# Performance work log

Measured on AMD Instinct MI355X. Metric: run time of the kernel, lower is better.

## Reference

```python
import jax, jax.numpy as jnp
import numpy as np

S_LEN = 1024; HIDDEN = 2048; VOCAB = 32000; DFF = 6144
NK = 8; NV = 16; DK = 128; DV = 128; CONV_K = 4
CONV_DIM = 2 * NK * DK + NV * DV  # 4096
NQ = 16; NKV = 2; HD = 128; MAX_KV = 4096; SP = 512; CHUNK = 64


def silu(x):
    return x * jax.nn.sigmoid(x)


def rmsnorm(x, w, eps=1e-6):
    xf = x.astype(jnp.float32)
    return (xf * jax.lax.rsqrt(jnp.mean(xf * xf, -1, keepdims=True) + eps)) * w


def gated_rmsnorm(x, z, w, eps=1e-6):
    xf = x.astype(jnp.float32) * silu(z.astype(jnp.float32))
    return (xf * jax.lax.rsqrt(jnp.mean(xf * xf, -1, keepdims=True) + eps)) * w


def rotate_half(x):
    a, b = jnp.split(x, 2, -1)
    return jnp.concatenate([-b, a], -1)


def chunk_gated_delta_rule(q, k, v, g, beta, init_state, chunk=CHUNK):
    # q,k: [B,S,H,Dk]; v: [B,S,H,Dv]; g,beta: [B,S,H]; init_state: [B,H,Dk,Dv]
    q = q / jnp.sqrt(jnp.sum(q * q, -1, keepdims=True) + 1e-6)  # qk l2norm
    k = k / jnp.sqrt(jnp.sum(k * k, -1, keepdims=True) + 1e-6)
    tr = lambda x: x.transpose(0, 2, 1, 3).astype(jnp.float32)
    q, k, v = tr(q), tr(k), tr(v)
    g = g.transpose(0, 2, 1).astype(jnp.float32)
    beta = beta.transpose(0, 2, 1).astype(jnp.float32)
    B, H, S, Dk = q.shape
    Dv = v.shape[-1]
    N = S // chunk  # S is a multiple of chunk here (no padding needed)
    q = q * Dk ** -0.5
    rc = lambda x: x.reshape(B, H, N, chunk, x.shape[-1])
    q, k, v = rc(q), rc(k), rc(v)
    g = jnp.cumsum(g.reshape(B, H, N, chunk), -1)  # cumulative log-decay within chunk
    beta = beta.reshape(B, H, N, chunk)
    kb = k * beta[..., None]
    vb = v * beta[..., None]
    ii = jnp.arange(chunk)
    lower = ii[:, None] >= ii[None, :]
    strict = ii[:, None] > ii[None, :]
    decay = jnp.where(lower, jnp.exp(g[..., :, None] - g[..., None, :]), 0.0)
    # strictly-lower A; T = (I - A)^{-1} (exact triangular solve == converged Neumann series)
    A = -jnp.where(strict, jnp.einsum('bhnik,bhnjk->bhnij', kb, k) * decay, 0.0)
    eye = jnp.eye(chunk, dtype=jnp.float32)
    T = jax.scipy.linalg.solve_triangular(eye - A, jnp.broadcast_to(eye, A.shape), lower=True)
    w = jnp.einsum('bhnij,bhnjd->bhnid', T, vb)
    kc = jnp.einsum('bhnij,bhnjd->bhnid', T, kb * jnp.exp(g)[..., None])
    mv = lambda x: jnp.moveaxis(x, 2, 0)

    def step(state, xs):
        qi, ki, wi, kci, gi, di = xs
        attn = jnp.where(lower, jnp.einsum('bhik,bhjk->bhij', qi, ki) * di, 0.0)
        v_new = wi - jnp.einsum('bhik,bhkd->bhid', kci, state)
        out = jnp.einsum('bhik,bhkd->bhid', qi * jnp.exp(gi)[..., None], state) \
            + jnp.einsum('bhij,bhjd->bhid', attn, v_new)
        gl = gi[..., -1]
        kd = ki * jnp.exp(gl[..., None] - gi)[..., None]
        state = state * jnp.exp(gl)[..., None, None] + jnp.einsum('bhik,bhid->bhkd', kd, v_new)
        return state, out

    final, outs = jax.lax.scan(step, init_state.astype(jnp.float32),
                               (mv(q), mv(k), mv(w), mv(kc), mv(g), mv(decay)))
    out = jnp.moveaxis(outs, 0, 2).reshape(B, H, S, Dv).transpose(0, 2, 1, 3)  # [B,S,H,Dv]
    return out, final


def mlp(x, gw, uw, dw):
    return (silu(x @ gw) * (x @ uw)) @ dw


def model_forward(input_ids, start_pos, rope_cos, rope_sin, attn_mask, conv_state, rec_state,
                  key_cache, value_cache, embed_w, dl_ln_w, dl_qkv_w, conv_w, conv_b, dl_z_w,
                  dl_b_w, dl_a_w, A_log, dt_bias, dn_norm_w, dl_out_w, dl_post_ln_w, dl_gate_w,
                  dl_up_w, dl_down_w, al_ln_w, q_w, q_norm_w, k_w, k_norm_w, v_w, o_w,
                  al_post_ln_w, al_gate_w, al_up_w, al_down_w, final_norm_w, lm_head_w):
    B, S = input_ids.shape
    hidden = embed_w[input_ids]
    # ---------------- DeltaNet (linear attention) layer ----------------
    res = hidden
    x = rmsnorm(hidden, dl_ln_w)
    mixed = (x @ dl_qkv_w).transpose(0, 2, 1)             # [B, CONV_DIM, S]
    padded = jnp.concatenate([conv_state, mixed], -1)      # [B, CONV_DIM, K+S]
    L = padded.shape[-1] - (CONV_K - 1)
    conv = conv_b[:, None] + sum(conv_w[:, kk][:, None] * padded[:, :, kk:kk + L]
                                 for kk in range(CONV_K))  # depthwise conv1d
    mixed = silu(conv[:, :, -S:]).transpose(0, 2, 1)
    new_conv = padded[:, :, -CONV_K:]
    kd = NK * DK
    qq = mixed[..., :kd].reshape(B, S, NK, DK)
    kk_ = mixed[..., kd:2 * kd].reshape(B, S, NK, DK)
    vv = mixed[..., 2 * kd:].reshape(B, S, NV, DV)
    z = (x @ dl_z_w).reshape(B, S, NV, DV)
    beta = jax.nn.sigmoid(x @ dl_b_w)
    a = (x @ dl_a_w).astype(jnp.float32)
    g = -jnp.exp(A_log.astype(jnp.float32)) * jax.nn.softplus(a + dt_bias)
    rep = NV // NK
    qq = jnp.repeat(qq, rep, axis=2)
    kk_ = jnp.repeat(kk_, rep, axis=2)
    core, new_rec = chunk_gated_delta_rule(qq, kk_, vv, g, beta, rec_state)
    core = gated_rmsnorm(core.reshape(-1, DV), z.reshape(-1, DV), dn_norm_w).reshape(B, S, NV * DV)
    hidden = res + core @ dl_out_w
    hidden = hidden + mlp(rmsnorm(hidden, dl_post_ln_w), dl_gate_w, dl_up_w, dl_down_w)
    # ---------------- Full attention layer (gated GQA, KV-cache scatter) ----------------
    res = hidden
    x = rmsnorm(hidden, al_ln_w)
    qg = (x @ q_w).reshape(B, S, NQ, 2 * HD)
    query, gate = jnp.split(qg, 2, -1)
    gate = gate.reshape(B, S, NQ * HD)
    query = rmsnorm(query, q_norm_w).transpose(0, 2, 1, 3)               # [B,NQ,S,HD]
    key_new = rmsnorm((x @ k_w).reshape(B, S, NKV, HD), k_norm_w).transpose(0, 2, 1, 3)
    value_new = (x @ v_w).reshape(B, S, NKV, HD).transpose(0, 2, 1, 3)
    c = rope_cos[:, None]
    sn = rope_sin[:, None]
    query = query * c + rotate_half(query) * sn
    key_new = key_new * c + rotate_half(key_new) * sn
    new_kc = jax.lax.dynamic_update_slice(key_cache, key_new, (0, 0, start_pos, 0))
    new_vc = jax.lax.dynamic_update_slice(value_cache, value_new, (0, 0, start_pos, 0))
    ng = NQ // NKV
    k_rep = jnp.repeat(new_kc, ng, axis=1)
    v_rep = jnp.repeat(new_vc, ng, axis=1)
    scores = jnp.einsum('bhsd,bhtd->bhst', query, k_rep) * HD ** -0.5 + attn_mask
    probs = jax.nn.softmax(scores.astype(jnp.float32), -1).astype(query.dtype)
    ao = jnp.einsum('bhst,bhtd->bhsd', probs, v_rep).transpose(0, 2, 1, 3).reshape(B, S, NQ * HD)
    ao = ao * jax.nn.sigmoid(gate)
    hidden = res + ao @ o_w
    hidden = hidden + mlp(rmsnorm(hidden, al_post_ln_w), al_gate_w, al_up_w, al_down_w)
    logits = rmsnorm(hidden, final_norm_w) @ lm_head_w
    return logits, new_conv, new_rec, new_kc, new_vc


def setup_inputs():
    key = jax.random.key(0)
    ks = iter(jax.random.split(key, 64))
    def rn(shape, s=0.02):
        return jax.random.normal(next(ks), shape, jnp.float32) * s
    input_ids = jax.random.randint(next(ks), (1, S_LEN), 0, VOCAB)
    inv = 1.0 / (10000.0 ** (jnp.arange(0, HD, 2, dtype=jnp.float32) / HD))
    pos = jnp.arange(SP, SP + S_LEN, dtype=jnp.float32)
    fr = pos[:, None] * inv[None, :]
    emb = jnp.concatenate([fr, fr], -1)
    rope_cos = jnp.cos(emb)[None]
    rope_sin = jnp.sin(emb)[None]
    qpos = SP + jnp.arange(S_LEN)
    kpos = jnp.arange(MAX_KV)
    attn_mask = jnp.where(kpos[None, :] <= qpos[:, None], 0.0, -1e9).astype(jnp.float32)[None, None]
    return dict(
        input_ids=input_ids, seq_len=S_LEN, start_pos=SP,
        rope_cos=rope_cos, rope_sin=rope_sin, attn_mask=attn_mask,
        conv_state=rn((1, CONV_DIM, CONV_K), 1.0), rec_state=rn((1, NV, DK, DV), 1.0),
        key_cache=rn((1, NKV, MAX_KV, HD), 1.0), value_cache=rn((1, NKV, MAX_KV, HD), 1.0),
        embed_w=rn((VOCAB, HIDDEN)), dl_ln_w=jnp.ones(HIDDEN),
        dl_qkv_w=rn((HIDDEN, CONV_DIM)), conv_w=rn((CONV_DIM, CONV_K), 0.3),
        conv_b=rn((CONV_DIM,)), dl_z_w=rn((HIDDEN, NV * DV)),
        dl_b_w=rn((HIDDEN, NV)), dl_a_w=rn((HIDDEN, NV)),
        A_log=jnp.log(jnp.linspace(1.0, 8.0, NV)), dt_bias=rn((NV,), 0.1),
        dn_norm_w=jnp.ones(DV), dl_out_w=rn((NV * DV, HIDDEN)),
        dl_post_ln_w=jnp.ones(HIDDEN), dl_gate_w=rn((HIDDEN, DFF)),
        dl_up_w=rn((HIDDEN, DFF)), dl_down_w=rn((DFF, HIDDEN)),
        al_ln_w=jnp.ones(HIDDEN), q_w=rn((HIDDEN, NQ * HD * 2)), q_norm_w=jnp.ones(HD),
        k_w=rn((HIDDEN, NKV * HD)), k_norm_w=jnp.ones(HD), v_w=rn((HIDDEN, NKV * HD)),
        o_w=rn((NQ * HD, HIDDEN)), al_post_ln_w=jnp.ones(HIDDEN),
        al_gate_w=rn((HIDDEN, DFF)), al_up_w=rn((HIDDEN, DFF)), al_down_w=rn((DFF, HIDDEN)),
        final_norm_w=jnp.ones(HIDDEN), lm_head_w=rn((HIDDEN, VOCAB)))


def reference(input_ids, seq_len, start_pos, rope_cos, rope_sin, attn_mask, conv_state,
              rec_state, key_cache, value_cache, embed_w, dl_ln_w, dl_qkv_w, conv_w, conv_b,
              dl_z_w, dl_b_w, dl_a_w, A_log, dt_bias, dn_norm_w, dl_out_w, dl_post_ln_w,
              dl_gate_w, dl_up_w, dl_down_w, al_ln_w, q_w, q_norm_w, k_w, k_norm_w, v_w, o_w,
              al_post_ln_w, al_gate_w, al_up_w, al_down_w, final_norm_w, lm_head_w):
    del seq_len  # unused in original forward body (padding bookkeeping only)
    return model_forward(input_ids, start_pos, rope_cos, rope_sin, attn_mask, conv_state,
                         rec_state, key_cache, value_cache, embed_w, dl_ln_w, dl_qkv_w, conv_w,
                         conv_b, dl_z_w, dl_b_w, dl_a_w, A_log, dt_bias, dn_norm_w, dl_out_w,
                         dl_post_ln_w, dl_gate_w, dl_up_w, dl_down_w, al_ln_w, q_w, q_norm_w,
                         k_w, k_norm_w, v_w, o_w, al_post_ln_w, al_gate_w, al_up_w, al_down_w,
                         final_norm_w, lm_head_w)
```

## Files before the change

### kernel.cpp

```cpp
#include <hip/hip_runtime.h>
#include <math.h>

#define S_LEN 1024
#define HIDN  2048
#define NVH   16
#define CDIM  4096
#define MAXKV 4096
#define SP    512

typedef __attribute__((ext_vector_type(4))) float f32x4v;
typedef _Float16 f16x8 __attribute__((ext_vector_type(8)));
typedef unsigned short ushort_t;

__device__ __forceinline__ unsigned int pack2h(float a, float b) {
  auto h = __builtin_amdgcn_cvt_pkrtz(a, b);
  return __builtin_bit_cast(unsigned int, h);
}
__device__ __forceinline__ ushort_t h16(float x) {
  auto v = __builtin_amdgcn_cvt_pkrtz(x, x);
  return (ushort_t)__builtin_bit_cast(unsigned int, v);
}

template<int TM, bool ACC, bool FS>
__global__ __launch_bounds__(256) void gemm_f16(const float* __restrict__ A,
    const float* A2, const float* __restrict__ B,
    float* __restrict__ C, int M, int N, int K) {
  constexpr int MI = TM / 32;
  constexpr int AF = TM / 8;
  __shared__ unsigned int Al[4][TM][4];
  __shared__ unsigned int Bl[4][128][4];
  const int tid = threadIdx.x;
  const int gm = M / TM;
  const int nwg = gridDim.x;
  const int q = nwg >> 3, r = nwg & 7;
  const int xcd = blockIdx.x & 7, ii = blockIdx.x >> 3;
  const int lin = (xcd < r) ? (xcd * (q + 1) + ii)
                            : (r * (q + 1) + (xcd - r) * q + ii);
  const int m0 = (lin % gm) * TM;
  const int n0 = (lin / gm) * 128;
  const int wave = tid >> 6, lane = tid & 63;
  const int wm = (wave >> 1) * (TM / 2), wn = (wave & 1) * 64;
  const int lr = lane & 15, lg = lane >> 4;
  const int am  = (TM == 128) ? (tid >> 1) : (tid >> 2);
  const int akb = (TM == 128) ? ((tid & 1) * 2) : (tid & 3);
  const int bn = tid & 127, bkb = (tid >> 7) * 2;
  const float* Ap  = A + (size_t)(m0 + am) * K + akb * 8;
  const float* A2p = A2 + (size_t)(m0 + am) * K + akb * 8;
  const float* Bp = B + (size_t)(bkb * 8) * N + n0 + bn;
  float ar[AF], ar2[FS ? AF : 1], br[16];
  f32x4v acc[MI][4];
  #pragma unroll
  for (int i = 0; i < MI; ++i)
    #pragma unroll
    for (int j = 0; j < 4; ++j)
      #pragma unroll
      for (int r2 = 0; r2 < 4; ++r2) acc[i][j][r2] = 0.f;
  const int NT = K >> 5;
  #pragma unroll
  for (int q2 = 0; q2 < AF / 4; ++q2)
    *(float4*)&ar[q2 * 4] = *(const float4*)(Ap + q2 * 4);
  if (FS) {
    #pragma unroll
    for (int q2 = 0; q2 < AF / 4; ++q2)
      *(float4*)&ar2[q2 * 4] = *(const float4*)(A2p + q2 * 4);
  }
  #pragma unroll
  for (int j = 0; j < 16; ++j) br[j] = Bp[(size_t)j * N];
  for (int t = 0; t < NT; ++t) {
    __syncthreads();
    float av[AF];
    #pragma unroll
    for (int u = 0; u < AF; ++u) {
      float g = ar[u];
      av[u] = FS ? (g / (1.f + expf(-g))) * ar2[u] : g;
    }
    *(uint4*)&Al[akb][am][0] = make_uint4(
        pack2h(av[0], av[1]), pack2h(av[2], av[3]),
        pack2h(av[4], av[5]), pack2h(av[6], av[7]));
    if (TM == 128) {
      *(uint4*)&Al[akb + 1][am][0] = make_uint4(
          pack2h(av[8], av[9]), pack2h(av[10], av[11]),
          pack2h(av[12], av[13]), pack2h(av[14], av[15]));
    }
    *(uint4*)&Bl[bkb][bn][0] = make_uint4(
        pack2h(br[0], br[1]), pack2h(br[2], br[3]),
        pack2h(br[4], br[5]), pack2h(br[6], br[7]));
    *(uint4*)&Bl[bkb + 1][bn][0] = make_uint4(
        pack2h(br[8], br[9]), pack2h(br[10], br[11]),
        pack2h(br[12], br[13]), pack2h(br[14], br[15]));
    if (t + 1 < NT) {
      Ap += 32; A2p += 32; Bp += (size_t)32 * N;
      #pragma unroll
      for (int q2 = 0; q2 < AF / 4; ++q2)
        *(float4*)&ar[q2 * 4] = *(const float4*)(Ap + q2 * 4);
      if (FS) {
        #pragma unroll
        for (int q2 = 0; q2 < AF / 4; ++q2)
          *(float4*)&ar2[q2 * 4] = *(const float4*)(A2p + q2 * 4);
      }
      #pragma unroll
      for (int j = 0; j < 16; ++j) br[j] = Bp[(size_t)j * N];
    }
    __syncthreads();
    f16x8 af[MI], bfr[4];
    #pragma unroll
    for (int mi = 0; mi < MI; ++mi)
      af[mi] = *(const f16x8*)&Al[lg][wm + mi * 16 + lr][0];
    #pragma unroll
    for (int ni = 0; ni < 4; ++ni)
      bfr[ni] = *(const f16x8*)&Bl[lg][wn + ni * 16 + lr][0];
    #pragma unroll
    for (int mi = 0; mi < MI; ++mi)
      #pragma unroll
      for (int ni = 0; ni < 4; ++ni)
        acc[mi][ni] = __builtin_amdgcn_mfma_f32_16x16x32_f16(
            af[mi], bfr[ni], acc[mi][ni], 0, 0, 0);
  }
  #pragma unroll
  for (int mi = 0; mi < MI; ++mi) {
    #pragma unroll
    for (int ni = 0; ni < 4; ++ni) {
      const int rr = m0 + wm + mi * 16 + lg * 4;
      const int cc = n0 + wn + ni * 16 + lr;
      #pragma unroll
      for (int r2 = 0; r2 < 4; ++r2) {
        float* cp = C + (size_t)(rr + r2) * N + cc;
        if (ACC) *cp += acc[mi][ni][r2];
        else     *cp = acc[mi][ni][r2];
      }
    }
  }
}

__global__ __launch_bounds__(256) void embed_k(const int* __restrict__ ids,
    const float* __restrict__ emb, float* __restrict__ hid) {
  int t = blockIdx.x * 256 + threadIdx.x;
  int s = t >> 9;
  int c4 = (t & 511) * 4;
  *(float4*)(hid + (size_t)s * HIDN + c4) =
      *(const float4*)(emb + (size_t)ids[s] * HIDN + c4);
}

__global__ __launch_bounds__(256) void rmsnorm_k(const float* __restrict__ in,
    const float* __restrict__ w, float* __restrict__ out) {
  const int row = blockIdx.x;
  const float* ip = in + (size_t)row * HIDN;
  float ss = 0.f;
  for (int c = threadIdx.x * 4; c < HIDN; c += 1024) {
    float4 v = *(const float4*)(ip + c);
    ss += v.x * v.x + v.y * v.y + v.z * v.z + v.w * v.w;
  }
  #pragma unroll
  for (int o = 32; o > 0; o >>= 1) ss += __shfl_down(ss, o, 64);
  __shared__ float sred[4];
  if ((threadIdx.x & 63) == 0) sred[threadIdx.x >> 6] = ss;
  __syncthreads();
  float tot = sred[0] + sred[1] + sred[2] + sred[3];
  float sc = 1.f / sqrtf(tot * (1.f / HIDN) + 1e-6f);
  for (int c = threadIdx.x * 4; c < HIDN; c += 1024) {
    float4 v = *(const float4*)(ip + c);
    float4 o = make_float4(v.x * sc * w[c], v.y * sc * w[c + 1],
                           v.z * sc * w[c + 2], v.w * sc * w[c + 3]);
    *(float4*)(out + (size_t)row * HIDN + c) = o;
  }
}

__global__ __launch_bounds__(256) void newconv_k(const float* __restrict__ mixed,
                                                 float* __restrict__ nc) {
  int t = blockIdx.x * 256 + threadIdx.x;
  int c = t >> 2, kk = t & 3;
  nc[t] = mixed[(size_t)(1020 + kk) * CDIM + c];
}

__global__ __launch_bounds__(256) void conv_k(const float* __restrict__ mixed,
    const float* __restrict__ cstate, const float* __restrict__ cw,
    const float* __restrict__ cb, float* __restrict__ convo) {
  int idx = blockIdx.x * 256 + threadIdx.x;
  int c = idx & (CDIM - 1);
  int s = idx >> 12;
  float acc = cb[c];
  #pragma unroll
  for (int kk = 0; kk < 4; ++kk) {
    int j = s + 1 + kk;
    float pv = (j < 4) ? cstate[c * 4 + j] : mixed[(size_t)(j - 4) * CDIM + c];
    acc = fmaf(cw[c * 4 + kk], pv, acc);
  }
  convo[(size_t)s * CDIM + c] = acc / (1.f + expf(-acc));
}

__global__ __launch_bounds__(128) void qknorm_k(const float* __restrict__ convo,
    float* __restrict__ qn, float* __restrict__ kn) {
  const int b = blockIdx.x;
  const int h8 = b & 7, s = b >> 3;
  const int d = threadIdx.x;
  float qv = convo[(size_t)s * CDIM + h8 * 128 + d];
  float kv = convo[(size_t)s * CDIM + 1024 + h8 * 128 + d];
  __shared__ float sred[4];
  float pq = qv * qv, pk = kv * kv;
  #pragma unroll
  for (int o = 32; o > 0; o >>= 1) { pq += __shfl_down(pq, o, 64); pk += __shfl_down(pk, o, 64); }
  if ((d & 63) == 0) { sred[d >> 6] = pq; sred[2 + (d >> 6)] = pk; }
  __syncthreads();
  float sq = sred[0] + sred[1], sk = sred[2] + sred[3];
  qn[((size_t)h8 * S_LEN + s) * 128 + d] = qv * (1.f / sqrtf(sq + 1e-6f)) * 0.08838834764831845f;
  kn[((size_t)h8 * S_LEN + s) * 128 + d] = kv * (1.f / sqrtf(sk + 1e-6f));
}

__global__ __launch_bounds__(256) void betag_k(const float* __restrict__ x,
    const float* __restrict__ bw, const float* __restrict__ aw,
    const float* __restrict__ A_log, const float* __restrict__ dt_bias,
    float* __restrict__ beta, float* __restrict__ g) {
  __shared__ float sx[2048];
  __shared__ float rb[16][17], ra[16][17];
  const int s = blockIdx.x;
  for (int c = threadIdx.x; c < HIDN; c += 256) sx[c] = x[(size_t)s * HIDN + c];
  __syncthreads();
  const int h = threadIdx.x & 15, part = threadIdx.x >> 4;
  float accb = 0.f, acca = 0.f;
  for (int j = 0; j < 128; ++j) {
    int k = part * 128 + j;
    float xv = sx[k];
    accb = fmaf(xv, bw[(size_t)k * 16 + h], accb);
    acca = fmaf(xv, aw[(size_t)k * 16 + h], acca);
  }
  rb[part][h] = accb; ra[part][h] = acca;
  __syncthreads();
  if (threadIdx.x < 16) {
    const int hh = threadIdx.x;
    float sb = 0.f, sa = 0.f;
    for (int p = 0; p < 16; ++p) { sb += rb[p][hh]; sa += ra[p][hh]; }
    beta[(size_t)s * 16 + hh] = 1.f / (1.f + expf(-sb));
    float aa = sa + dt_bias[hh];
    float sp = (aa > 20.f) ? aa : log1pf(expf(aa));
    g[(size_t)s * 16 + hh] = -expf(A_log[hh]) * sp;
  }
}

__global__ __launch_bounds__(256) void delta_phase1(
    const float* __restrict__ qn, const float* __restrict__ kn,
    const float* __restrict__ convo, const float* __restrict__ beta,
    const float* __restrict__ g,
    float* __restrict__ Wb, ushort_t* __restrict__ KC16,
    ushort_t* __restrict__ Q16, ushort_t* __restrict__ K16,
    ushort_t* __restrict__ ATT16, float* __restrict__ GCb) {
  __shared__ float sK[64][129];
  __shared__ float sV[64][129];
  __shared__ float sQ[64][129];
  __shared__ float sT[64][64];
  __shared__ float sgc[64], sbeta[64], seg[64], sEgl[64];
  const int blk = blockIdx.x;
  const int n = blk & 15, h = blk >> 4;
  const int hq = h >> 1;
  const int r0 = n * 64;
  const int tid = threadIdx.x;
  const size_t hn = (size_t)h * 16 + n;
  for (int t = tid; t < 2048; t += 256) {
    int i = t >> 5, c4 = (t & 31) * 4;
    float4 kv = *(const float4*)(kn + ((size_t)hq * S_LEN + r0 + i) * 128 + c4);
    float4 qv = *(const float4*)(qn + ((size_t)hq * S_LEN + r0 + i) * 128 + c4);
    float4 vv = *(const float4*)(convo + (size_t)(r0 + i) * CDIM + 2048 + h * 128 + c4);
    sK[i][c4+0]=kv.x; sK[i][c4+1]=kv.y; sK[i][c4+2]=kv.z; sK[i][c4+3]=kv.w;
    sQ[i][c4+0]=qv.x; sQ[i][c4+1]=qv.y; sQ[i][c4+2]=qv.z; sQ[i][c4+3]=qv.w;
    sV[i][c4+0]=vv.x; sV[i][c4+1]=vv.y; sV[i][c4+2]=vv.z; sV[i][c4+3]=vv.w;
  }
  if (tid < 64) sbeta[tid] = beta[(size_t)(r0 + tid) * NVH + h];
  __syncthreads();
  if (tid == 0) {
    float acc = 0.f;
    for (int i = 0; i < 64; ++i) { acc += g[(size_t)(r0 + i) * NVH + h]; sgc[i] = acc; }
  }
  __syncthreads();
  if (tid < 64) {
    seg[tid] = expf(sgc[tid]);
    sEgl[tid] = expf(sgc[63] - sgc[tid]);
  }
  {
    const int ty = tid >> 4, tx = tid & 15;
    float a[4][4] = {};
    #pragma unroll 4
    for (int k = 0; k < 128; ++k) {
      float kr[4], kc_[4];
      #pragma unroll
      for (int di = 0; di < 4; ++di) kr[di] = sK[ty * 4 + di][k];
      #pragma unroll
      for (int dj = 0; dj < 4; ++dj) kc_[dj] = sK[tx * 4 + dj][k];
      #pragma unroll
      for (int di = 0; di < 4; ++di)
        #pragma unroll
        for (int dj = 0; dj < 4; ++dj)
          a[di][dj] = fmaf(kr[di], kc_[dj], a[di][dj]);
    }
    #pragma unroll
    for (int di = 0; di < 4; ++di) {
      int i = ty * 4 + di;
      #pragma unroll
      for (int dj = 0; dj < 4; ++dj) {
        int j = tx * 4 + dj;
        float v;
        if (i > j) v = sbeta[i] * a[di][dj] * expf(sgc[i] - sgc[j]);
        else v = (i == j) ? 1.f : 0.f;
        sT[i][j] = v;
      }
    }
  }
  __syncthreads();
  if (tid < 64) {
    const int c = tid;
    for (int i = 1; i < 64; ++i) {
      if (c <= i) {
        float acc = (c == i) ? 1.f : 0.f;
        for (int j = c; j < i; ++j) acc -= sT[i][j] * sT[j][c];
        sT[i][c] = acc;
      }
    }
  }
  __syncthreads();
  for (int t = tid; t < 1024; t += 256) {
    int i = t >> 4, dg = (t & 15) * 8;
    float aw[8] = {}, ak[8] = {};
    for (int j = 0; j <= i; ++j) {
      float tv = sT[i][j] * sbeta[j];
      float te = tv * seg[j];
      #pragma unroll
      for (int u = 0; u < 8; ++u) {
        aw[u] = fmaf(tv, sV[j][dg + u], aw[u]);
        ak[u] = fmaf(te, sK[j][dg + u], ak[u]);
      }
    }
    float* wp = Wb + (hn * 64 + i) * 128 + dg;
    *(float4*)wp = make_float4(aw[0], aw[1], aw[2], aw[3]);
    *(float4*)(wp + 4) = make_float4(aw[4], aw[5], aw[6], aw[7]);
    uint4 kc = make_uint4(pack2h(-ak[0], -ak[1]), pack2h(-ak[2], -ak[3]),
                          pack2h(-ak[4], -ak[5]), pack2h(-ak[6], -ak[7]));
    *(uint4*)(KC16 + hn * 8192 + (dg >> 3) * 512 + i * 8) = kc;
  }
  for (int t = tid; t < 1024; t += 256) {
    int i = t >> 4, dg = (t & 15) * 8;
    float e = seg[i];
    uint4 qv = make_uint4(
        pack2h(sQ[i][dg] * e, sQ[i][dg + 1] * e),
        pack2h(sQ[i][dg + 2] * e, sQ[i][dg + 3] * e),
        pack2h(sQ[i][dg + 4] * e, sQ[i][dg + 5] * e),
        pack2h(sQ[i][dg + 6] * e, sQ[i][dg + 7] * e));
    *(uint4*)(Q16 + hn * 8192 + (dg >> 3) * 512 + i * 8) = qv;
  }
  for (int t = tid; t < 1024; t += 256) {
    int kv = t & 127, ib = t >> 7;
    int i0 = ib * 8;
    uint4 kk2 = make_uint4(
        pack2h(sK[i0 + 0][kv] * sEgl[i0 + 0], sK[i0 + 1][kv] * sEgl[i0 + 1]),
        pack2h(sK[i0 + 2][kv] * sEgl[i0 + 2], sK[i0 + 3][kv] * sEgl[i0 + 3]),
        pack2h(sK[i0 + 4][kv] * sEgl[i0 + 4], sK[i0 + 5][kv] * sEgl[i0 + 5]),
        pack2h(sK[i0 + 6][kv] * sEgl[i0 + 6], sK[i0 + 7][kv] * sEgl[i0 + 7]));
    *(uint4*)(K16 + hn * 8192 + ib * 1024 + kv * 8) = kk2;
  }
  __syncthreads();
  {
    const int ty = tid >> 4, tx = tid & 15;
    float a[4][4] = {};
    #pragma unroll 4
    for (int k = 0; k < 128; ++k) {
      float qr[4], kc_[4];
      #pragma unroll
      for (int di = 0; di < 4; ++di) qr[di] = sQ[ty * 4 + di][k];
      #pragma unroll
      for (int dj = 0; dj < 4; ++dj) kc_[dj] = sK[tx * 4 + dj][k];
      #pragma unroll
      for (int di = 0; di < 4; ++di)
        #pragma unroll
        for (int dj = 0; dj < 4; ++dj)
          a[di][dj] = fmaf(qr[di], kc_[dj], a[di][dj]);
    }
    #pragma unroll
    for (int di = 0; di < 4; ++di) {
      int i = ty * 4 + di;
      #pragma unroll
      for (int dj = 0; dj < 4; ++dj) {
        int j = tx * 4 + dj;
        float v = 0.f;
        if (i >= j) v = a[di][dj] * expf(sgc[i] - sgc[j]);
        sT[i][j] = v;
      }
    }
  }
  __syncthreads();
  for (int t = tid; t < 512; t += 256) {
    int i = t >> 3, jb = t & 7;
    const float* ap = &sT[i][jb * 8];
    uint4 av = make_uint4(pack2h(ap[0], ap[1]), pack2h(ap[2], ap[3]),
                          pack2h(ap[4], ap[5]), pack2h(ap[6], ap[7]));
    *(uint4*)(ATT16 + hn * 4096 + jb * 512 + i * 8) = av;
  }
  if (tid < 64) GCb[hn * 64 + tid] = sgc[tid];
}

__global__ __launch_bounds__(256) void delta_phase2(
    const ushort_t* __restrict__ KC16, const ushort_t* __restrict__ Q16,
    const ushort_t* __restrict__ K16, const ushort_t* __restrict__ ATT16,
    const float* __restrict__ Wb, const float* __restrict__ GCb,
    const float* __restrict__ rec_state,
    float* __restrict__ core, float* __restrict__ new_rec) {
  __shared__ uint4 bufKC[1024];
  __shared__ uint4 bufQ[1024];
  __shared__ uint4 bufK[1024];
  __shared__ uint4 bufA[512];
  __shared__ uint4 bufS[512];
  __shared__ uint4 bufV[256];
  ushort_t* sKC = (ushort_t*)bufKC;
  ushort_t* sQ6 = (ushort_t*)bufQ;
  ushort_t* sK6 = (ushort_t*)bufK;
  ushort_t* sAT = (ushort_t*)bufA;
  ushort_t* sS  = (ushort_t*)bufS;
  ushort_t* sVn = (ushort_t*)bufV;
  const int h = blockIdx.x >> 2, ds = blockIdx.x & 3;
  const int d0 = ds * 32;
  const int tid = threadIdx.x;
  const int w = tid >> 6;
  const int lane = tid & 63, lr = lane & 15, lg = lane >> 4;
  const int rowS0 = w * 32;
  f32x4v aS[2][2];
  #pragma unroll
  for (int tm = 0; tm < 2; ++tm)
    #pragma unroll
    for (int tn = 0; tn < 2; ++tn)
      #pragma unroll
      for (int r = 0; r < 4; ++r) {
        int row = rowS0 + tm * 16 + lg * 4 + r;
        int col = tn * 16 + lr;
        aS[tm][tn][r] = rec_state[((size_t)h * 128 + row) * 128 + d0 + col];
      }
  for (int n = 0; n < 16; ++n) {
    const size_t hn = (size_t)h * 16 + n;
    const uint4* pKC = (const uint4*)(KC16 + hn * 8192);
    const uint4* pQ  = (const uint4*)(Q16  + hn * 8192);
    const uint4* pK  = (const uint4*)(K16  + hn * 8192);
    const uint4* pA  = (const uint4*)(ATT16 + hn * 4096);
    uint4 stKC[4], stQ[4], stK[4], stA[2];
    #pragma unroll
    for (int u = 0; u < 4; ++u) {
      stKC[u] = pKC[tid + u * 256];
      stQ[u]  = pQ[tid + u * 256];
      stK[u]  = pK[tid + u * 256];
    }
    #pragma unroll
    for (int u = 0; u < 2; ++u) stA[u] = pA[tid + u * 256];
    const float egl = expf(GCb[hn * 64 + 63]);
    float wseed[2][4];
    #pragma unroll
    for (int tn = 0; tn < 2; ++tn)
      #pragma unroll
      for (int r = 0; r < 4; ++r)
        wseed[tn][r] = Wb[(hn * 64 + (w * 16 + lg * 4 + r)) * 128 + d0 + tn * 16 + lr];
    #pragma unroll
    for (int tm = 0; tm < 2; ++tm)
      #pragma unroll
      for (int tn = 0; tn < 2; ++tn)
        #pragma unroll
        for (int r = 0; r < 4; ++r) {
          int row = rowS0 + tm * 16 + lg * 4 + r;
          int col = tn * 16 + lr;
          sS[(row >> 3) * 256 + col * 8 + (row & 7)] = h16(aS[tm][tn][r]);
        }
    #pragma unroll
    for (int u = 0; u < 4; ++u) {
      bufKC[tid + u * 256] = stKC[u];
      bufQ[tid + u * 256]  = stQ[u];
      bufK[tid + u * 256]  = stK[u];
    }
    #pragma unroll
    for (int u = 0; u < 2; ++u) bufA[tid + u * 256] = stA[u];
    __syncthreads();
    f32x4v aV[2];
    #pragma unroll
    for (int tn = 0; tn < 2; ++tn)
      #pragma unroll
      for (int r = 0; r < 4; ++r) aV[tn][r] = wseed[tn][r];
    #pragma unroll
    for (int c = 0; c < 4; ++c) {
      f16x8 a = *(const f16x8*)&sKC[((c * 4 + lg) * 64 + w * 16 + lr) * 8];
      #pragma unroll
      for (int tn = 0; tn < 2; ++tn) {
        f16x8 b = *(const f16x8*)&sS[((c * 4 + lg) * 32 + tn * 16 + lr) * 8];
        aV[tn] = __builtin_amdgcn_mfma_f32_16x16x32_f16(a, b, aV[tn], 0, 0, 0);
      }
    }
    #pragma unroll
    for (int tn = 0; tn < 2; ++tn)
      #pragma unroll
      for (int r = 0; r < 4; ++r) {
        int row = w * 16 + lg * 4 + r;
        int col = tn * 16 + lr;
        sVn[(row >> 3) * 256 + col * 8 + (row & 7)] = h16(aV[tn][r]);
      }
    __syncthreads();
    f32x4v aO[2];
    #pragma unroll
    for (int tn = 0; tn < 2; ++tn)
      #pragma unroll
      for (int r = 0; r < 4; ++r) aO[tn][r] = 0.f;
    #pragma unroll
    for (int c = 0; c < 4; ++c) {
      f16x8 a = *(const f16x8*)&sQ6[((c * 4 + lg) * 64 + w * 16 + lr) * 8];
      #pragma unroll
      for (int tn = 0; tn < 2; ++tn) {
        f16x8 b = *(const f16x8*)&sS[((c * 4 + lg) * 32 + tn * 16 + lr) * 8];
        aO[tn] = __builtin_amdgcn_mfma_f32_16x16x32_f16(a, b, aO[tn], 0, 0, 0);
      }
    }
    #pragma unroll
    for (int c = 0; c < 2; ++c) {
      f16x8 a = *(const f16x8*)&sAT[((c * 4 + lg) * 64 + w * 16 + lr) * 8];
      #pragma unroll
      for (int tn = 0; tn < 2; ++tn) {
        f16x8 b = *(const f16x8*)&sVn[((c * 4 + lg) * 32 + tn * 16 + lr) * 8];
        aO[tn] = __builtin_amdgcn_mfma_f32_16x16x32_f16(a, b, aO[tn], 0, 0, 0);
      }
    }
    #pragma unroll
    for (int tn = 0; tn < 2; ++tn)
      #pragma unroll
      for (int r = 0; r < 4; ++r) {
        int row = w * 16 + lg * 4 + r;
        core[(size_t)(n * 64 + row) * HIDN + h * 128 + d0 + tn * 16 + lr] = aO[tn][r];
      }
    #pragma unroll
    for (int tm = 0; tm < 2; ++tm)
      #pragma unroll
      for (int tn = 0; tn < 2; ++tn)
        #pragma unroll
        for (int r = 0; r < 4; ++r) aS[tm][tn][r] *= egl;
    #pragma unroll
    for (int tm = 0; tm < 2; ++tm) {
      #pragma unroll
      for (int c = 0; c < 2; ++c) {
        f16x8 a = *(const f16x8*)&sK6[((c * 4 + lg) * 128 + rowS0 + tm * 16 + lr) * 8];
        #pragma unroll
        for (int tn = 0; tn < 2; ++tn) {
          f16x8 b = *(const f16x8*)&sVn[((c * 4 + lg) * 32 + tn * 16 + lr) * 8];
          aS[tm][tn] = __builtin_amdgcn_mfma_f32_16x16x32_f16(a, b, aS[tm][tn], 0, 0, 0);
        }
      }
    }
    __syncthreads();
  }
  #pragma unroll
  for (int tm = 0; tm < 2; ++tm)
    #pragma unroll
    for (int tn = 0; tn < 2; ++tn)
      #pragma unroll
      for (int r = 0; r < 4; ++r) {
        int row = rowS0 + tm * 16 + lg * 4 + r;
        int col = tn * 16 + lr;
        new_rec[((size_t)h * 128 + row) * 128 + d0 + col] = aS[tm][tn][r];
      }
}

__global__ __launch_bounds__(128) void gatedrms_k(float* __restrict__ core,
    const float* __restrict__ z, const float* __restrict__ w) {
  const int b = blockIdx.x;
  const int h = b & 15, s = b >> 4;
  const int d = threadIdx.x;
  size_t idx = (size_t)s * HIDN + h * 128 + d;
  float cv = core[idx], zv = z[idx];
  float xf = cv * (zv / (1.f + expf(-zv)));
  __shared__ float sred[2];
  float ps = xf * xf;
  #pragma unroll
  for (int o = 32; o > 0; o >>= 1) ps += __shfl_down(ps, o, 64);
  if ((d & 63) == 0) sred[d >> 6] = ps;
  __syncthreads();
  float ss = sred[0] + sred[1];
  core[idx] = xf * (1.f / sqrtf(ss * (1.f / 128.f) + 1e-6f)) * w[d];
}

__global__ __launch_bounds__(128) void qrope_k(const float* __restrict__ qg,
    const float* __restrict__ qnw, const float* __restrict__ cosb,
    const float* __restrict__ sinb, float* __restrict__ qhat,
    float* __restrict__ agate) {
  const int b = blockIdx.x;
  const int h = b & 15, s = b >> 4;
  const int d = threadIdx.x;
  float qv = qg[(size_t)s * 4096 + h * 256 + d];
  float gv = qg[(size_t)s * 4096 + h * 256 + 128 + d];
  __shared__ float sred[2];
  float ps = qv * qv;
  #pragma unroll
  for (int o = 32; o > 0; o >>= 1) ps += __shfl_down(ps, o, 64);
  if ((d & 63) == 0) sred[d >> 6] = ps;
  __syncthreads();
  float ss = sred[0] + sred[1];
  float qn_ = qv * (1.f / sqrtf(ss * (1.f / 128.f) + 1e-6f)) * qnw[d];
  __shared__ float tmp[128];
  tmp[d] = qn_;
  __syncthreads();
  float other = tmp[d ^ 64];
  float rh = (d < 64) ? -other : other;
  float c = cosb[(size_t)s * 128 + d];
  float sn = sinb[(size_t)s * 128 + d];
  qhat[((size_t)h * S_LEN + s) * 128 + d] = qn_ * c + rh * sn;
  agate[(size_t)s * HIDN + h * 128 + d] = gv;
}

__global__ __launch_bounds__(128) void kvrope_k(const float* __restrict__ kraw,
    const float* __restrict__ vraw, const float* __restrict__ knw,
    const float* __restrict__ cosb, const float* __restrict__ sinb,
    float* __restrict__ kcache, float* __restrict__ vcache) {
  const int b = blockIdx.x;
  const int h2 = b & 1, s = b >> 1;
  const int d = threadIdx.x;
  float kv = kraw[(size_t)s * 256 + h2 * 128 + d];
  __shared__ float sred[2];
  float ps = kv * kv;
  #pragma unroll
  for (int o = 32; o > 0; o >>= 1) ps += __shfl_down(ps, o, 64);
  if ((d & 63) == 0) sred[d >> 6] = ps;
  __syncthreads();
  float ss = sred[0] + sred[1];
  float kn_ = kv * (1.f / sqrtf(ss * (1.f / 128.f) + 1e-6f)) * knw[d];
  __shared__ float tmp[128];
  tmp[d] = kn_;
  __syncthreads();
  float other = tmp[d ^ 64];
  float rh = (d < 64) ? -other : other;
  size_t row = (size_t)h2 * MAXKV + SP + s;
  kcache[row * 128 + d] = kn_ * cosb[(size_t)s * 128 + d] + rh * sinb[(size_t)s * 128 + d];
  vcache[row * 128 + d] = vraw[(size_t)s * 256 + h2 * 128 + d];
}

__global__ __launch_bounds__(256) void attn_k(const float* __restrict__ qhat,
    const float* __restrict__ kcache, const float* __restrict__ vcache,
    const float* __restrict__ agate, float* __restrict__ ao) {
  __shared__ unsigned int Ql[16][64][4];
  __shared__ unsigned int Kl[16][64][4];
  __shared__ unsigned int Vl[8][128][4];
  __shared__ unsigned int Pl[8][64][4];
  const int h = blockIdx.x >> 4, qb = blockIdx.x & 15;
  const int hkv = h >> 3;
  const int tid = threadIdx.x;
  const int wave = tid >> 6, lane = tid & 63;
  const int lr = lane & 15, lg = lane >> 4;
  const float SCALE = 0.08838834764831845f;
  const float* Qb = qhat + ((size_t)h * S_LEN + qb * 64) * 128;
  #pragma unroll
  for (int it = 0; it < 4; ++it) {
    int tt = tid + it * 256;
    int row = tt >> 4, kb = tt & 15;
    float4 a = *(const float4*)(Qb + row * 128 + kb * 8);
    float4 b = *(const float4*)(Qb + row * 128 + kb * 8 + 4);
    *(uint4*)&Ql[kb][row][0] = make_uint4(
        pack2h(a.x * SCALE, a.y * SCALE), pack2h(a.z * SCALE, a.w * SCALE),
        pack2h(b.x * SCALE, b.y * SCALE), pack2h(b.z * SCALE, b.w * SCALE));
  }
  float m_run[4], l_run[4];
  #pragma unroll
  for (int r = 0; r < 4; ++r) { m_run[r] = -3.0e38f; l_run[r] = 0.f; }
  f32x4v accO[8];
  #pragma unroll
  for (int nd = 0; nd < 8; ++nd)
    #pragma unroll
    for (int r = 0; r < 4; ++r) accO[nd][r] = 0.f;
  const int ntiles = 9 + qb;
  for (int kt = 0; kt < ntiles; ++kt) {
    __syncthreads();
    const float* Kb = kcache + ((size_t)hkv * MAXKV + kt * 64) * 128;
    const float* Vb = vcache + ((size_t)hkv * MAXKV + kt * 64) * 128;
    #pragma unroll
    for (int it = 0; it < 4; ++it) {
      int tt = tid + it * 256;
      int row = tt >> 4, kb = tt & 15;
      float4 a = *(const float4*)(Kb + row * 128 + kb * 8);
      float4 b = *(const float4*)(Kb + row * 128 + kb * 8 + 4);
      *(uint4*)&Kl[kb][row][0] = make_uint4(
          pack2h(a.x, a.y), pack2h(a.z, a.w), pack2h(b.x, b.y), pack2h(b.z, b.w));
    }
    #pragma unroll
    for (int it = 0; it < 4; ++it) {
      int tt = tid + it * 256;
      int key = tt >> 4, dg = tt & 15;
      float4 a = *(const float4*)(Vb + key * 128 + dg * 8);
      float4 b = *(const float4*)(Vb + key * 128 + dg * 8 + 4);
      _Float16* vp = (_Float16*)Vl;
      int base = (key >> 3) * 1024 + (key & 7);
      vp[base + (dg * 8 + 0) * 8] = (_Float16)a.x;
      vp[base + (dg * 8 + 1) * 8] = (_Float16)a.y;
      vp[base + (dg * 8 + 2) * 8] = (_Float16)a.z;
      vp[base + (dg * 8 + 3) * 8] = (_Float16)a.w;
      vp[base + (dg * 8 + 4) * 8] = (_Float16)b.x;
      vp[base + (dg * 8 + 5) * 8] = (_Float16)b.y;
      vp[base + (dg * 8 + 6) * 8] = (_Float16)b.z;
      vp[base + (dg * 8 + 7) * 8] = (_Float16)b.w;
    }
    __syncthreads();
    f32x4v accS[4];
    #pragma unroll
    for (int ni = 0; ni < 4; ++ni)
      #pragma unroll
      for (int r = 0; r < 4; ++r) accS[ni][r] = 0.f;
    #pragma unroll
    for (int c = 0; c < 4; ++c) {
      f16x8 aq = *(const f16x8*)&Ql[c * 4 + lg][wave * 16 + lr][0];
      #pragma unroll
      for (int ni = 0; ni < 4; ++ni) {
        f16x8 bk = *(const f16x8*)&Kl[c * 4 + lg][ni * 16 + lr][0];
        accS[ni] = __builtin_amdgcn_mfma_f32_16x16x32_f16(aq, bk, accS[ni], 0, 0, 0);
      }
    }
    const bool boundary = (kt == ntiles - 1);
    float alpha[4];
    #pragma unroll
    for (int r = 0; r < 4; ++r) {
      const int qrow = wave * 16 + lg * 4 + r;
      float tm = -3.0e38f;
      #pragma unroll
      for (int ni = 0; ni < 4; ++ni) {
        if (boundary && (ni * 16 + lr) > qrow) accS[ni][r] = -3.0e38f;
        tm = fmaxf(tm, accS[ni][r]);
      }
      tm = fmaxf(tm, __shfl_xor(tm, 1, 64));
      tm = fmaxf(tm, __shfl_xor(tm, 2, 64));
      tm = fmaxf(tm, __shfl_xor(tm, 4, 64));
      tm = fmaxf(tm, __shfl_xor(tm, 8, 64));
      float mnew = fmaxf(m_run[r], tm);
      alpha[r] = expf(m_run[r] - mnew);
      m_run[r] = mnew;
      float ls = 0.f;
      #pragma unroll
      for (int ni = 0; ni < 4; ++ni) {
        float p = expf(accS[ni][r] - mnew);
        accS[ni][r] = p;
        ls += p;
      }
      ls += __shfl_xor(ls, 1, 64);
      ls += __shfl_xor(ls, 2, 64);
      ls += __shfl_xor(ls, 4, 64);
      ls += __shfl_xor(ls, 8, 64);
      l_run[r] = l_run[r] * alpha[r] + ls;
    }
    {
      _Float16* pp = (_Float16*)Pl;
      #pragma unroll
      for (int ni = 0; ni < 4; ++ni) {
        int key = ni * 16 + lr;
        int base = (key >> 3) * 512 + (key & 7);
        #pragma unroll
        for (int r = 0; r < 4; ++r) {
          int q = wave * 16 + lg * 4 + r;
          pp[base + q * 8] = (_Float16)accS[ni][r];
        }
      }
    }
    #pragma unroll
    for (int nd = 0; nd < 8; ++nd)
      #pragma unroll
      for (int r = 0; r < 4; ++r) accO[nd][r] *= alpha[r];
    #pragma unroll
    for (int c2 = 0; c2 < 2; ++c2) {
      f16x8 ap = *(const f16x8*)&Pl[c2 * 4 + lg][wave * 16 + lr][0];
      #pragma unroll
      for (int nd = 0; nd < 8; ++nd) {
        f16x8 bv = *(const f16x8*)&Vl[c2 * 4 + lg][nd * 16 + lr][0];
        accO[nd] = __builtin_amdgcn_mfma_f32_16x16x32_f16(ap, bv, accO[nd], 0, 0, 0);
      }
    }
  }
  #pragma unroll
  for (int r = 0; r < 4; ++r) {
    const int s = qb * 64 + wave * 16 + lg * 4 + r;
    const float inv = 1.f / l_run[r];
    #pragma unroll
    for (int nd = 0; nd < 8; ++nd) {
      int d = nd * 16 + lr;
      float gv = agate[(size_t)s * HIDN + h * 128 + d];
      ao[(size_t)s * HIDN + h * 128 + d] = accO[nd][r] * inv * (1.f / (1.f + expf(-gv)));
    }
  }
}

static inline void gemm128(const float* A, const float* B, float* C,
                           int M, int N, int K, bool acc, hipStream_t st) {
  dim3 g((N / 128) * (M / 128));
  if (acc) hipLaunchKernelGGL((gemm_f16<128, true,  false>), g, dim3(256), 0, st, A, A, B, C, M, N, K);
  else     hipLaunchKernelGGL((gemm_f16<128, false, false>), g, dim3(256), 0, st, A, A, B, C, M, N, K);
}
static inline void gemm64(const float* A, const float* B, float* C,
                          int M, int N, int K, bool acc, hipStream_t st) {
  dim3 g((N / 128) * (M / 64));
  if (acc) hipLaunchKernelGGL((gemm_f16<64, true,  false>), g, dim3(256), 0, st, A, A, B, C, M, N, K);
  else     hipLaunchKernelGGL((gemm_f16<64, false, false>), g, dim3(256), 0, st, A, A, B, C, M, N, K);
}
static inline void gemm_dn(const float* G, const float* U, const float* B, float* C,
                           int M, int N, int K, hipStream_t st) {
  dim3 g((N / 128) * (M / 64));
  hipLaunchKernelGGL((gemm_f16<64, true, true>), g, dim3(256), 0, st, G, U, B, C, M, N, K);
}

extern "C" void kernel_launch(void* const* d_in, const int* in_sizes, int n_in,
                              void* d_out, int out_size, void* d_ws, size_t ws_size,
                              hipStream_t stream) {
  (void)in_sizes; (void)n_in; (void)out_size; (void)ws_size;
  const int*   ids         = (const int*)  d_in[0];
  const float* rope_cos    = (const float*)d_in[3];
  const float* rope_sin    = (const float*)d_in[4];
  const float* conv_state  = (const float*)d_in[6];
  const float* rec_state   = (const float*)d_in[7];
  const float* key_cache   = (const float*)d_in[8];
  const float* value_cache = (const float*)d_in[9];
  const float* embed_w     = (const float*)d_in[10];
  const float* dl_ln_w     = (const float*)d_in[11];
  const float* dl_qkv_w    = (const float*)d_in[12];
  const float* conv_w      = (const float*)d_in[13];
  const float* conv_b      = (const float*)d_in[14];
  const float* dl_z_w      = (const float*)d_in[15];
  const float* dl_b_w      = (const float*)d_in[16];
  const float* dl_a_w      = (const float*)d_in[17];
  const float* A_log       = (const float*)d_in[18];
  const float* dt_bias     = (const float*)d_in[19];
  const float* dn_norm_w   = (const float*)d_in[20];
  const float* dl_out_w    = (const float*)d_in[21];
  const float* dl_post_ln  = (const float*)d_in[22];
  const float* dl_gate_w   = (const float*)d_in[23];
  const float* dl_up_w     = (const float*)d_in[24];
  const float* dl_down_w   = (const float*)d_in[25];
  const float* al_ln_w     = (const float*)d_in[26];
  const float* q_w         = (const float*)d_in[27];
  const float* q_norm_w    = (const float*)d_in[28];
  const float* k_w         = (const float*)d_in[29];
  const float* k_norm_w    = (const float*)d_in[30];
  const float* v_w         = (const float*)d_in[31];
  const float* o_w         = (const float*)d_in[32];
  const float* al_post_ln  = (const float*)d_in[33];
  const float* al_gate_w   = (const float*)d_in[34];
  const float* al_up_w     = (const float*)d_in[35];
  const float* al_down_w   = (const float*)d_in[36];
  const float* final_norm  = (const float*)d_in[37];
  const float* lm_head_w   = (const float*)d_in[38];

  float* out = (float*)d_out;
  float* logits   = out;
  float* new_conv = out + 32768000;
  float* new_rec  = out + 32784384;
  float* new_kc   = out + 33046528;
  float* new_vc   = out + 34095104;

  float* A_mixed = logits;
  float* A_convo = logits + 4194304;
  float* A_z     = logits + 8388608;
  float* A_qn    = logits + 10485760;
  float* A_kn    = logits + 11534336;
  float* A_w     = logits + 12582912;
  float* A_kc    = logits + 14680064;
  float* A_att   = logits + 16777216;
  float* A_gc    = logits + 17825792;
  float* A_core  = logits + 17842176;
  float* A_big0  = logits + 19939328;
  float* A_big1  = logits + 26230784;
  float* A_qhat  = A_big1;
  float* A_gate  = A_big1 + 2097152;
  float* A_ao    = A_big1 + 4194304;
  float* A_kraw  = A_mixed;
  float* A_vraw  = A_mixed + 262144;

  ushort_t* KC16  = (ushort_t*)A_kc;
  ushort_t* K16   = (ushort_t*)A_kc + 2097152;
  ushort_t* Q16   = (ushort_t*)A_att;
  ushort_t* ATT16 = (ushort_t*)A_big0;

  float* ws     = (float*)d_ws;
  float* W_hid  = ws;
  float* W_x    = ws + 2097152;
  float* W_beta = ws + 4194304;
  float* W_g    = ws + 4210688;

  hipLaunchKernelGGL(embed_k, dim3(2048), dim3(256), 0, stream, ids, embed_w, W_hid);
  hipLaunchKernelGGL(rmsnorm_k, dim3(1024), dim3(256), 0, stream, W_hid, dl_ln_w, W_x);
  gemm128(W_x, dl_qkv_w, A_mixed, 1024, 4096, 2048, false, stream);
  hipLaunchKernelGGL(newconv_k, dim3(64), dim3(256), 0, stream, A_mixed, new_conv);
  hipLaunchKernelGGL(conv_k, dim3(16384), dim3(256), 0, stream,
                     A_mixed, conv_state, conv_w, conv_b, A_convo);
  gemm64(W_x, dl_z_w, A_z, 1024, 2048, 2048, false, stream);
  hipLaunchKernelGGL(betag_k, dim3(1024), dim3(256), 0, stream,
                     W_x, dl_b_w, dl_a_w, A_log, dt_bias, W_beta, W_g);
  hipLaunchKernelGGL(qknorm_k, dim3(8192), dim3(128), 0, stream, A_convo, A_qn, A_kn);
  hipLaunchKernelGGL(delta_phase1, dim3(256), dim3(256), 0, stream,
                     A_qn, A_kn, A_convo, W_beta, W_g,
                     A_w, KC16, Q16, K16, ATT16, A_gc);
  hipLaunchKernelGGL(delta_phase2, dim3(64), dim3(256), 0, stream,
                     KC16, Q16, K16, ATT16, A_w, A_gc, rec_state, A_core, new_rec);
  hipLaunchKernelGGL(gatedrms_k, dim3(16384), dim3(128), 0, stream, A_core, A_z, dn_norm_w);
  gemm64(A_core, dl_out_w, W_hid, 1024, 2048, 2048, true, stream);
  hipLaunchKernelGGL(rmsnorm_k, dim3(1024), dim3(256), 0, stream, W_hid, dl_post_ln, W_x);
  gemm64(W_x, dl_gate_w, A_big0, 1024, 6144, 2048, false, stream);
  gemm64(W_x, dl_up_w,   A_big1, 1024, 6144, 2048, false, stream);
  gemm_dn(A_big0, A_big1, dl_down_w, W_hid, 1024, 2048, 6144, stream);
  hipLaunchKernelGGL(rmsnorm_k, dim3(1024), dim3(256), 0, stream, W_hid, al_ln_w, W_x);
  gemm128(W_x, q_w, A_big0, 1024, 4096, 2048, false, stream);
  hipLaunchKernelGGL(qrope_k, dim3(16384), dim3(128), 0, stream,
                     A_big0, q_norm_w, rope_cos, rope_sin, A_qhat, A_gate);
  gemm64(W_x, k_w, A_kraw, 1024, 256, 2048, false, stream);
  gemm64(W_x, v_w, A_vraw, 1024, 256, 2048, false, stream);
  hipMemcpyAsync(new_kc, key_cache,   (size_t)2 * MAXKV * 128 * 4, hipMemcpyDeviceToDevice, stream);
  hipMemcpyAsync(new_vc, value_cache, (size_t)2 * MAXKV * 128 * 4, hipMemcpyDeviceToDevice, stream);
  hipLaunchKernelGGL(kvrope_k, dim3(2048), dim3(128), 0, stream,
                     A_kraw, A_vraw, k_norm_w, rope_cos, rope_sin, new_kc, new_vc);
  hipLaunchKernelGGL(attn_k, dim3(256), dim3(256), 0, stream,
                     A_qhat, new_kc, new_vc, A_gate, A_ao);
  gemm64(A_ao, o_w, W_hid, 1024, 2048, 2048, true, stream);
  hipLaunchKernelGGL(rmsnorm_k, dim3(1024), dim3(256), 0, stream, W_hid, al_post_ln, W_x);
  gemm64(W_x, al_gate_w, A_big0, 1024, 6144, 2048, false, stream);
  gemm64(W_x, al_up_w,   A_big1, 1024, 6144, 2048, false, stream);
  gemm_dn(A_big0, A_big1, al_down_w, W_hid, 1024, 2048, 6144, stream);
  hipLaunchKernelGGL(rmsnorm_k, dim3(1024), dim3(256), 0, stream, W_hid, final_norm, W_x);
  gemm128(W_x, lm_head_w, logits, 1024, 32000, 2048, false, stream);
}
```

Baseline: 1.733 ms.

## Double GEMM K-tile to 64 and pre-convert KV cache to fp16 tiles

```diff
diff --git a/kernel.cpp b/kernel.cpp
--- a/kernel.cpp
+++ b/kernel.cpp
@@ -20,15 +20,21 @@
   auto v = __builtin_amdgcn_cvt_pkrtz(x, x);
   return (ushort_t)__builtin_bit_cast(unsigned int, v);
 }
+__device__ __forceinline__ void gload16(const void* g, void* l) {
+  __builtin_amdgcn_global_load_lds(
+      (const __attribute__((address_space(1))) void*)(g),
+      (__attribute__((address_space(3))) void*)(l), 16, 0, 0);
+}
 
 template<int TM, bool ACC, bool FS>
 __global__ __launch_bounds__(256) void gemm_f16(const float* __restrict__ A,
     const float* A2, const float* __restrict__ B,
     float* __restrict__ C, int M, int N, int K) {
   constexpr int MI = TM / 32;
-  constexpr int AF = TM / 8;
-  __shared__ unsigned int Al[4][TM][4];
-  __shared__ unsigned int Bl[4][128][4];
+  constexpr int AG = TM / 32;
+  constexpr int AF = AG * 8;
+  __shared__ unsigned int Al[8][TM][4];
+  __shared__ unsigned int Bl[8][128][4];
   const int tid = threadIdx.x;
   const int gm = M / TM;
   const int nwg = gridDim.x;
@@ -42,12 +48,12 @@
   const int wm = (wave >> 1) * (TM / 2), wn = (wave & 1) * 64;
   const int lr = lane & 15, lg = lane >> 4;
   const int am  = (TM == 128) ? (tid >> 1) : (tid >> 2);
-  const int akb = (TM == 128) ? ((tid & 1) * 2) : (tid & 3);
-  const int bn = tid & 127, bkb = (tid >> 7) * 2;
+  const int akb = (TM == 128) ? ((tid & 1) * 4) : ((tid & 3) * 2);
+  const int bn = tid & 127, bkb = (tid >> 7) * 4;
   const float* Ap  = A + (size_t)(m0 + am) * K + akb * 8;
   const float* A2p = A2 + (size_t)(m0 + am) * K + akb * 8;
   const float* Bp = B + (size_t)(bkb * 8) * N + n0 + bn;
-  float ar[AF], ar2[FS ? AF : 1], br[16];
+  float ar[AF], ar2[FS ? AF : 1], br[32];
   f32x4v acc[MI][4];
   #pragma unroll
   for (int i = 0; i < MI; ++i)
@@ -55,7 +61,7 @@
     for (int j = 0; j < 4; ++j)
       #pragma unroll
       for (int r2 = 0; r2 < 4; ++r2) acc[i][j][r2] = 0.f;
-  const int NT = K >> 5;
+  const int NT = K >> 6;
   #pragma unroll
   for (int q2 = 0; q2 < AF / 4; ++q2)
     *(float4*)&ar[q2 * 4] = *(const float4*)(Ap + q2 * 4);
@@ -65,7 +71,7 @@
       *(float4*)&ar2[q2 * 4] = *(const float4*)(A2p + q2 * 4);
   }
   #pragma unroll
-  for (int j = 0; j < 16; ++j) br[j] = Bp[(size_t)j * N];
+  for (int j = 0; j < 32; ++j) br[j] = Bp[(size_t)j * N];
   for (int t = 0; t < NT; ++t) {
     __syncthreads();
     float av[AF];
@@ -74,22 +80,22 @@
       float g = ar[u];
       av[u] = FS ? (g / (1.f + expf(-g))) * ar2[u] : g;
     }
-    *(uint4*)&Al[akb][am][0] = make_uint4(
-        pack2h(av[0], av[1]), pack2h(av[2], av[3]),
-        pack2h(av[4], av[5]), pack2h(av[6], av[7]));
-    if (TM == 128) {
-      *(uint4*)&Al[akb + 1][am][0] = make_uint4(
-          pack2h(av[8], av[9]), pack2h(av[10], av[11]),
-          pack2h(av[12], av[13]), pack2h(av[14], av[15]));
-    }
-    *(uint4*)&Bl[bkb][bn][0] = make_uint4(
-        pack2h(br[0], br[1]), pack2h(br[2], br[3]),
-        pack2h(br[4], br[5]), pack2h(br[6], br[7]));
-    *(uint4*)&Bl[bkb + 1][bn][0] = make_uint4(
-        pack2h(br[8], br[9]), pack2h(br[10], br[11]),
-        pack2h(br[12], br[13]), pack2h(br[14], br[15]));
+    #pragma unroll
+    for (int g2 = 0; g2 < AG; ++g2)
+      *(uint4*)&Al[akb + g2][am][0] = make_uint4(
+          pack2h(av[g2 * 8 + 0], av[g2 * 8 + 1]),
+          pack2h(av[g2 * 8 + 2], av[g2 * 8 + 3]),
+          pack2h(av[g2 * 8 + 4], av[g2 * 8 + 5]),
+          pack2h(av[g2 * 8 + 6], av[g2 * 8 + 7]));
+    #pragma unroll
+    for (int g2 = 0; g2 < 4; ++g2)
+      *(uint4*)&Bl[bkb + g2][bn][0] = make_uint4(
+          pack2h(br[g2 * 8 + 0], br[g2 * 8 + 1]),
+          pack2h(br[g2 * 8 + 2], br[g2 * 8 + 3]),
+          pack2h(br[g2 * 8 + 4], br[g2 * 8 + 5]),
+          pack2h(br[g2 * 8 + 6], br[g2 * 8 + 7]));
     if (t + 1 < NT) {
-      Ap += 32; A2p += 32; Bp += (size_t)32 * N;
+      Ap += 64; A2p += 64; Bp += (size_t)64 * N;
       #pragma unroll
       for (int q2 = 0; q2 < AF / 4; ++q2)
         *(float4*)&ar[q2 * 4] = *(const float4*)(Ap + q2 * 4);
@@ -99,22 +105,25 @@
           *(float4*)&ar2[q2 * 4] = *(const float4*)(A2p + q2 * 4);
       }
       #pragma unroll
-      for (int j = 0; j < 16; ++j) br[j] = Bp[(size_t)j * N];
+      for (int j = 0; j < 32; ++j) br[j] = Bp[(size_t)j * N];
     }
     __syncthreads();
-    f16x8 af[MI], bfr[4];
-    #pragma unroll
-    for (int mi = 0; mi < MI; ++mi)
-      af[mi] = *(const f16x8*)&Al[lg][wm + mi * 16 + lr][0];
-    #pragma unroll
-    for (int ni = 0; ni < 4; ++ni)
-      bfr[ni] = *(const f16x8*)&Bl[lg][wn + ni * 16 + lr][0];
-    #pragma unroll
-    for (int mi = 0; mi < MI; ++mi)
+    #pragma unroll
+    for (int c = 0; c < 2; ++c) {
+      f16x8 af[MI], bfr[4];
+      #pragma unroll
+      for (int mi = 0; mi < MI; ++mi)
+        af[mi] = *(const f16x8*)&Al[c * 4 + lg][wm + mi * 16 + lr][0];
       #pragma unroll
       for (int ni = 0; ni < 4; ++ni)
-        acc[mi][ni] = __builtin_amdgcn_mfma_f32_16x16x32_f16(
-            af[mi], bfr[ni], acc[mi][ni], 0, 0, 0);
+        bfr[ni] = *(const f16x8*)&Bl[c * 4 + lg][wn + ni * 16 + lr][0];
+      #pragma unroll
+      for (int mi = 0; mi < MI; ++mi)
+        #pragma unroll
+        for (int ni = 0; ni < 4; ++ni)
+          acc[mi][ni] = __builtin_amdgcn_mfma_f32_16x16x32_f16(
+              af[mi], bfr[ni], acc[mi][ni], 0, 0, 0);
+    }
   }
   #pragma unroll
   for (int mi = 0; mi < MI; ++mi) {
@@ -627,8 +636,44 @@
   vcache[row * 128 + d] = vraw[(size_t)s * 256 + h2 * 128 + d];
 }
 
+__global__ __launch_bounds__(256) void kv16_k(const float* __restrict__ kc,
+    const float* __restrict__ vc, ushort_t* __restrict__ KV16) {
+  const int b = blockIdx.x;
+  const int kt = b % 24, h2 = b / 24;
+  const int tid = threadIdx.x;
+  const float* Kb = kc + ((size_t)h2 * MAXKV + kt * 64) * 128;
+  const float* Vb = vc + ((size_t)h2 * MAXKV + kt * 64) * 128;
+  ushort_t* Ko = KV16 + ((size_t)h2 * 24 + kt) * 8192;
+  ushort_t* Vo = KV16 + 393216 + ((size_t)h2 * 24 + kt) * 8192;
+  #pragma unroll
+  for (int it = 0; it < 4; ++it) {
+    int tt = tid + it * 256;
+    int row = tt >> 4, kb = tt & 15;
+    float4 a = *(const float4*)(Kb + row * 128 + kb * 8);
+    float4 c = *(const float4*)(Kb + row * 128 + kb * 8 + 4);
+    *(uint4*)(Ko + ((size_t)kb * 64 + row) * 8) = make_uint4(
+        pack2h(a.x, a.y), pack2h(a.z, a.w), pack2h(c.x, c.y), pack2h(c.z, c.w));
+  }
+  #pragma unroll
+  for (int it = 0; it < 4; ++it) {
+    int tt = tid + it * 256;
+    int key = tt >> 4, dg = tt & 15;
+    float4 a = *(const float4*)(Vb + key * 128 + dg * 8);
+    float4 c = *(const float4*)(Vb + key * 128 + dg * 8 + 4);
+    int base = (key >> 3) * 1024 + (key & 7);
+    Vo[base + (dg * 8 + 0) * 8] = h16(a.x);
+    Vo[base + (dg * 8 + 1) * 8] = h16(a.y);
+    Vo[base + (dg * 8 + 2) * 8] = h16(a.z);
+    Vo[base + (dg * 8 + 3) * 8] = h16(a.w);
+    Vo[base + (dg * 8 + 4) * 8] = h16(c.x);
+    Vo[base + (dg * 8 + 5) * 8] = h16(c.y);
+    Vo[base + (dg * 8 + 6) * 8] = h16(c.z);
+    Vo[base + (dg * 8 + 7) * 8] = h16(c.w);
+  }
+}
+
 __global__ __launch_bounds__(256) void attn_k(const float* __restrict__ qhat,
-    const float* __restrict__ kcache, const float* __restrict__ vcache,
+    const ushort_t* __restrict__ KV16,
     const float* __restrict__ agate, float* __restrict__ ao) {
   __shared__ unsigned int Ql[16][64][4];
   __shared__ unsigned int Kl[16][64][4];
@@ -662,33 +707,13 @@
   const int ntiles = 9 + qb;
   for (int kt = 0; kt < ntiles; ++kt) {
     __syncthreads();
-    const float* Kb = kcache + ((size_t)hkv * MAXKV + kt * 64) * 128;
-    const float* Vb = vcache + ((size_t)hkv * MAXKV + kt * 64) * 128;
-    #pragma unroll
-    for (int it = 0; it < 4; ++it) {
-      int tt = tid + it * 256;
-      int row = tt >> 4, kb = tt & 15;
-      float4 a = *(const float4*)(Kb + row * 128 + kb * 8);
-      float4 b = *(const float4*)(Kb + row * 128 + kb * 8 + 4);
-      *(uint4*)&Kl[kb][row][0] = make_uint4(
-          pack2h(a.x, a.y), pack2h(a.z, a.w), pack2h(b.x, b.y), pack2h(b.z, b.w));
-    }
-    #pragma unroll
-    for (int it = 0; it < 4; ++it) {
-      int tt = tid + it * 256;
-      int key = tt >> 4, dg = tt & 15;
-      float4 a = *(const float4*)(Vb + key * 128 + dg * 8);
-      float4 b = *(const float4*)(Vb + key * 128 + dg * 8 + 4);
-      _Float16* vp = (_Float16*)Vl;
-      int base = (key >> 3) * 1024 + (key & 7);
-      vp[base + (dg * 8 + 0) * 8] = (_Float16)a.x;
-      vp[base + (dg * 8 + 1) * 8] = (_Float16)a.y;
-      vp[base + (dg * 8 + 2) * 8] = (_Float16)a.z;
-      vp[base + (dg * 8 + 3) * 8] = (_Float16)a.w;
-      vp[base + (dg * 8 + 4) * 8] = (_Float16)b.x;
-      vp[base + (dg * 8 + 5) * 8] = (_Float16)b.y;
-      vp[base + (dg * 8 + 6) * 8] = (_Float16)b.z;
-      vp[base + (dg * 8 + 7) * 8] = (_Float16)b.w;
+    const ushort_t* Ks = KV16 + ((size_t)hkv * 24 + kt) * 8192;
+    const ushort_t* Vs = KV16 + 393216 + ((size_t)hkv * 24 + kt) * 8192;
+    #pragma unroll
+    for (int i2 = 0; i2 < 4; ++i2) {
+      int c = wave * 4 + i2;
+      gload16(Ks + (size_t)c * 512 + lane * 8, (char*)Kl + c * 1024);
+      gload16(Vs + (size_t)c * 512 + lane * 8, (char*)Vl + c * 1024);
     }
     __syncthreads();
     f32x4v accS[4];
@@ -864,6 +889,7 @@
   ushort_t* K16   = (ushort_t*)A_kc + 2097152;
   ushort_t* Q16   = (ushort_t*)A_att;
   ushort_t* ATT16 = (ushort_t*)A_big0;
+  ushort_t* KV16  = (ushort_t*)(A_big0 + 4194304);
 
   float* ws     = (float*)d_ws;
   float* W_hid  = ws;
@@ -902,8 +928,9 @@
   hipMemcpyAsync(new_vc, value_cache, (size_t)2 * MAXKV * 128 * 4, hipMemcpyDeviceToDevice, stream);
   hipLaunchKernelGGL(kvrope_k, dim3(2048), dim3(128), 0, stream,
                      A_kraw, A_vraw, k_norm_w, rope_cos, rope_sin, new_kc, new_vc);
+  hipLaunchKernelGGL(kv16_k, dim3(48), dim3(256), 0, stream, new_kc, new_vc, KV16);
   hipLaunchKernelGGL(attn_k, dim3(256), dim3(256), 0, stream,
-                     A_qhat, new_kc, new_vc, A_gate, A_ao);
+                     A_qhat, KV16, A_gate, A_ao);
   gemm64(A_ao, o_w, W_hid, 1024, 2048, 2048, true, stream);
   hipLaunchKernelGGL(rmsnorm_k, dim3(1024), dim3(256), 0, stream, W_hid, al_post_ln, W_x);
   gemm64(W_x, al_gate_w, A_big0, 1024, 6144, 2048, false, stream);
```

Result: no change. 1.746 ms (+0.7%).
